# Kernel optimization log

Measured on AMD Instinct MI355X. Metric: run time of the kernel, lower is better.

The kernel has to match this reference:

```python
import jax, jax.numpy as jnp
import numpy as np

B, L, E, H = 4096, 200, 64, 128

def setup_inputs() -> dict:
    key = jax.random.key(0)
    k1, k2, k3, k4, k5, k6, k7 = jax.random.split(key, 7)
    behavior_emb = jax.random.normal(k1, (B, L, E), dtype=jnp.float32)
    target_emb = jax.random.normal(k2, (B, 1, E), dtype=jnp.float32)
    seq_len = jax.random.randint(k3, (B,), 0, 200)
    # attention MLP params: Linear(4E, H), Linear(H, 1)
    W1 = jax.random.normal(k4, (4 * E, H), dtype=jnp.float32) / np.sqrt(4 * E)
    b1 = jnp.zeros((H,), dtype=jnp.float32)
    W2 = jax.random.normal(k5, (H, 1), dtype=jnp.float32) / np.sqrt(H)
    b2 = jnp.zeros((1,), dtype=jnp.float32)
    return {"behavior_emb": behavior_emb, "target_emb": target_emb,
            "seq_len": seq_len, "W1": W1, "b1": b1, "W2": W2, "b2": b2}

def reference(behavior_emb, target_emb, seq_len, W1, b1, W2, b2):
    b, l, e = behavior_emb.shape
    t = jnp.broadcast_to(target_emb, (b, l, e))  # [B,L,E]
    # concat(behavior, target, behavior*target, behavior-target) -> [B,L,4E]
    feat = jnp.concatenate([behavior_emb, t, behavior_emb * t, behavior_emb - t], axis=-1)
    h = jax.nn.relu(jnp.einsum('blf,fh->blh', feat, W1) + b1)  # dropout = identity (eval)
    att = (jnp.einsum('blh,ho->blo', h, W2) + b2)[..., 0]      # [B,L]
    mask = jnp.arange(l)[None, :] < seq_len[:, None]           # [B,L]
    att = jnp.where(mask, att, -1e9)
    att = jax.nn.softmax(att, axis=-1)
    weighted_emb = jnp.einsum('bl,ble->be', att, behavior_emb)  # [B,E]
    return weighted_emb
```

## Files before the change

kernel.cpp:

```cpp
#include <hip/hip_runtime.h>
#include <hip/hip_bf16.h>

typedef __attribute__((ext_vector_type(8))) __bf16 bf16x8;
typedef __attribute__((ext_vector_type(4))) __bf16 bf16x4;
typedef __attribute__((ext_vector_type(4))) float  f32x4;

#define L_SEQ 200
#define LPAD  208

__global__ __launch_bounds__(256) void din_attn_kernel(
    const float* __restrict__ behavior,
    const float* __restrict__ target,
    const int*   __restrict__ seqlen,
    const float* __restrict__ W1,
    const float* __restrict__ b1,
    const float* __restrict__ W2,
    float* __restrict__ out)
{
    __shared__ __align__(16) __bf16 Xbf[LPAD * 64];
    __shared__ __align__(16) __bf16 Wb[128 * 64];
    __shared__ float t_s[64];
    __shared__ float tb_s[128];
    __shared__ float att_s[L_SEQ];
    __shared__ float red_s[8];
    __shared__ float part_s[4 * 64];

    const int b    = blockIdx.x;
    const int tid  = threadIdx.x;
    const int lane = tid & 63;
    const int wave = tid >> 6;

    if (tid < 64) t_s[tid] = target[b * 64 + tid];
    __syncthreads();

    {
        const int col = tid & 127;
        const int kh  = tid >> 7;
        #pragma unroll
        for (int kk = 0; kk < 32; ++kk) {
            const int k = kh * 32 + kk;
            float w = W1[k * 128 + col] + W1[(192 + k) * 128 + col]
                    + t_s[k] * W1[(128 + k) * 128 + col];
            Wb[col * 64 + (k ^ ((col & 7) << 3))] = (__bf16)w;
        }
    }
    if (tid < 128) {
        float acc = b1[tid];
        #pragma unroll 4
        for (int e = 0; e < 64; ++e)
            acc += t_s[e] * (W1[(64 + e) * 128 + tid] - W1[(192 + e) * 128 + tid]);
        tb_s[tid] = acc;
    }
    {
        const float4* Xg = (const float4*)(behavior + (size_t)b * L_SEQ * 64);
        for (int q = tid; q < L_SEQ * 16; q += 256) {
            const int row = q >> 4;
            const int j   = q & 15;
            float4 v = Xg[q];
            const int idx = row * 64 + ((j * 4) ^ ((row & 7) << 3));
            bf16x4 u = { (__bf16)v.x, (__bf16)v.y, (__bf16)v.z, (__bf16)v.w };
            *(bf16x4*)&Xbf[idx] = u;
        }
        for (int q = tid; q < 8 * 64; q += 256) {
            const int row = L_SEQ + (q >> 6);
            const int e   = q & 63;
            Xbf[row * 64 + (e ^ ((row & 7) << 3))] = (__bf16)0.0f;
        }
    }
    __syncthreads();

    {
        bf16x8 bfrag[8][2];
        float tb_l[8], w2_l[8];
        #pragma unroll
        for (int nt = 0; nt < 8; ++nt) {
            const int col = nt * 16 + (lane & 15);
            #pragma unroll
            for (int ks = 0; ks < 2; ++ks) {
                const int k0 = ks * 32 + (lane >> 4) * 8;
                bfrag[nt][ks] = *(const bf16x8*)&Wb[col * 64 + (k0 ^ ((col & 7) << 3))];
            }
            tb_l[nt] = tb_s[col];
            w2_l[nt] = W2[col];
        }
        const f32x4 zero = {0.f, 0.f, 0.f, 0.f};
        for (int tile = wave; tile < 13; tile += 4) {
            const int row = tile * 16 + (lane & 15);
            const int k0  = (lane >> 4) * 8;
            const int sw  = (row & 7) << 3;
            bf16x8 a0 = *(const bf16x8*)&Xbf[row * 64 + (k0 ^ sw)];
            bf16x8 a1 = *(const bf16x8*)&Xbf[row * 64 + ((k0 + 32) ^ sw)];
            f32x4 acc[8];
            #pragma unroll
            for (int nt = 0; nt < 8; ++nt) acc[nt] = zero;
            #pragma unroll
            for (int nt = 0; nt < 8; ++nt) {
                acc[nt] = __builtin_amdgcn_mfma_f32_16x16x32_bf16(a0, bfrag[nt][0], acc[nt], 0, 0, 0);
                acc[nt] = __builtin_amdgcn_mfma_f32_16x16x32_bf16(a1, bfrag[nt][1], acc[nt], 0, 0, 0);
            }
            float s[4] = {0.f, 0.f, 0.f, 0.f};
            #pragma unroll
            for (int nt = 0; nt < 8; ++nt) {
                #pragma unroll
                for (int i = 0; i < 4; ++i)
                    s[i] += fmaxf(acc[nt][i] + tb_l[nt], 0.f) * w2_l[nt];
            }
            #pragma unroll
            for (int i = 0; i < 4; ++i) {
                float v = s[i];
                v += __shfl_xor(v, 1, 64);
                v += __shfl_xor(v, 2, 64);
                v += __shfl_xor(v, 4, 64);
                v += __shfl_xor(v, 8, 64);
                s[i] = v;
            }
            if ((lane & 15) == 0) {
                const int r = tile * 16 + (lane >> 4) * 4;
                #pragma unroll
                for (int i = 0; i < 4; ++i)
                    if (r + i < L_SEQ) att_s[r + i] = s[i];
            }
        }
    }
    __syncthreads();

    {
        const int sl = seqlen[b];
        float val = -INFINITY;
        if (tid < L_SEQ) val = (tid < sl) ? att_s[tid] : -1e9f;
        float m = val;
        #pragma unroll
        for (int d = 1; d < 64; d <<= 1) m = fmaxf(m, __shfl_xor(m, d, 64));
        if (lane == 0) red_s[wave] = m;
        __syncthreads();
        m = fmaxf(fmaxf(red_s[0], red_s[1]), fmaxf(red_s[2], red_s[3]));
        float p = (tid < L_SEQ) ? __expf(val - m) : 0.f;
        float sum = p;
        #pragma unroll
        for (int d = 1; d < 64; d <<= 1) sum += __shfl_xor(sum, d, 64);
        if (lane == 0) red_s[4 + wave] = sum;
        __syncthreads();
        sum = red_s[4] + red_s[5] + red_s[6] + red_s[7];
        const float winv = 1.0f / sum;
        if (tid < L_SEQ) att_s[tid] = p * winv;
    }
    __syncthreads();

    {
        float acc = 0.f;
        for (int l = wave; l < L_SEQ; l += 4)
            acc += att_s[l] * (float)Xbf[l * 64 + (lane ^ ((l & 7) << 3))];
        part_s[wave * 64 + lane] = acc;
    }
    __syncthreads();
    if (tid < 64)
        out[(size_t)b * 64 + tid] =
            part_s[tid] + part_s[64 + tid] + part_s[128 + tid] + part_s[192 + tid];
}

extern "C" void kernel_launch(void* const* d_in, const int* in_sizes, int n_in,
                              void* d_out, int out_size, void* d_ws, size_t ws_size,
                              hipStream_t stream) {
    (void)n_in; (void)out_size; (void)d_ws; (void)ws_size;
    const float* behavior = (const float*)d_in[0];
    const float* target   = (const float*)d_in[1];
    const int*   seqlen   = (const int*)d_in[2];
    const float* W1       = (const float*)d_in[3];
    const float* b1       = (const float*)d_in[4];
    const float* W2       = (const float*)d_in[5];
    float* out = (float*)d_out;
    const int B = in_sizes[2];
    din_attn_kernel<<<dim3(B), dim3(256), 0, stream>>>(behavior, target, seqlen, W1, b1, W2, out);
}
```

Before: 389.3 us.

## Precompute batch-independent weight fragments and per-batch bias in separate setup kernels

Moves the per-block folding of W1 into a shared bf16 weight matrix out to a one-time setup kernel that writes MFMA-ready fragments. The target-dependent bias is computed by a second batched setup kernel. The main kernel now forms the behavior*target operand on the fly, running a K=128 GEMM split across waves by column tile, with per-wave partial scores summed in shared memory. This removes redundant W1 reads and the shared weight buffer from every block, which should raise occupancy. The cost is two extra launches, a workspace dependency, more MFMA work per tile, and bf16 rounding of the product and bias.

New measurement: 334.2 us. -14.1%, faster.

```diff
diff --git a/kernel.cpp b/kernel.cpp
--- a/kernel.cpp
+++ b/kernel.cpp
@@ -8,58 +8,105 @@
 #define L_SEQ 200
 #define LPAD  208
 
-__global__ __launch_bounds__(256) void din_attn_kernel(
+__global__ void setup_bc(const float* __restrict__ W1, __bf16* __restrict__ Bc) {
+    const int idx = blockIdx.x * 256 + threadIdx.x;
+    const int j  = idx & 7;
+    const int c  = (idx >> 3) & 15;
+    const int kq = (idx >> 7) & 3;
+    const int ks = (idx >> 9) & 3;
+    const int ct = idx >> 11;
+    const int k   = ks * 32 + kq * 8 + j;
+    const int col = ct * 16 + c;
+    float v;
+    if (k < 64) v = W1[k * 128 + col] + W1[(192 + k) * 128 + col];
+    else        v = W1[(128 + (k - 64)) * 128 + col];
+    Bc[idx] = (__bf16)v;
+}
+
+__global__ __launch_bounds__(256) void setup_tb(
+    const float* __restrict__ target, const float* __restrict__ W1,
+    const float* __restrict__ b1, __bf16* __restrict__ TB)
+{
+    __shared__ float Wbd[64][128];
+    __shared__ float Ts[16][64];
+    const int tid = threadIdx.x;
+    const int b0  = blockIdx.x * 16;
+    for (int q = tid; q < 64 * 128; q += 256) {
+        const int e = q >> 7, c = q & 127;
+        Wbd[e][c] = W1[(64 + e) * 128 + c] - W1[(192 + e) * 128 + c];
+    }
+    for (int q = tid; q < 16 * 64; q += 256) {
+        const int bb = q >> 6, e = q & 63;
+        Ts[bb][e] = target[(size_t)(b0 + bb) * 64 + e];
+    }
+    __syncthreads();
+    const int bb = tid >> 4;
+    const int c0 = (tid & 15) * 8;
+    float acc[8];
+    #pragma unroll
+    for (int r = 0; r < 8; ++r) acc[r] = b1[c0 + r];
+    for (int e = 0; e < 64; ++e) {
+        const float tv = Ts[bb][e];
+        #pragma unroll
+        for (int r = 0; r < 8; ++r) acc[r] += tv * Wbd[e][c0 + r];
+    }
+    #pragma unroll
+    for (int r = 0; r < 8; ++r)
+        TB[(size_t)(b0 + bb) * 128 + c0 + r] = (__bf16)acc[r];
+}
+
+__global__ __launch_bounds__(256, 4) void din_main(
     const float* __restrict__ behavior,
     const float* __restrict__ target,
     const int*   __restrict__ seqlen,
-    const float* __restrict__ W1,
-    const float* __restrict__ b1,
     const float* __restrict__ W2,
+    const __bf16* __restrict__ Bc,
+    const __bf16* __restrict__ TB,
     float* __restrict__ out)
 {
     __shared__ __align__(16) __bf16 Xbf[LPAD * 64];
-    __shared__ __align__(16) __bf16 Wb[128 * 64];
-    __shared__ float t_s[64];
-    __shared__ float tb_s[128];
-    __shared__ float att_s[L_SEQ];
+    __shared__ float att_part[4][LPAD];
+    __shared__ float att_s[LPAD];
     __shared__ float red_s[8];
     __shared__ float part_s[4 * 64];
 
     const int b    = blockIdx.x;
     const int tid  = threadIdx.x;
     const int lane = tid & 63;
-    const int wave = tid >> 6;
-
-    if (tid < 64) t_s[tid] = target[b * 64 + tid];
-    __syncthreads();
-
-    {
-        const int col = tid & 127;
-        const int kh  = tid >> 7;
-        #pragma unroll
-        for (int kk = 0; kk < 32; ++kk) {
-            const int k = kh * 32 + kk;
-            float w = W1[k * 128 + col] + W1[(192 + k) * 128 + col]
-                    + t_s[k] * W1[(128 + k) * 128 + col];
-            Wb[col * 64 + (k ^ ((col & 7) << 3))] = (__bf16)w;
-        }
-    }
-    if (tid < 128) {
-        float acc = b1[tid];
-        #pragma unroll 4
-        for (int e = 0; e < 64; ++e)
-            acc += t_s[e] * (W1[(64 + e) * 128 + tid] - W1[(192 + e) * 128 + tid]);
-        tb_s[tid] = acc;
-    }
+    const int w    = tid >> 6;
+    const int kq   = lane >> 4;
+    const int c16  = lane & 15;
+
+    bf16x8 bfrag[2][4];
+    #pragma unroll
+    for (int i = 0; i < 2; ++i) {
+        const int ct = 2 * w + i;
+        #pragma unroll
+        for (int ks = 0; ks < 4; ++ks)
+            bfrag[i][ks] = *(const bf16x8*)(Bc + ((ct * 4 + ks) * 4 + kq) * 128 + c16 * 8);
+    }
+    float tf0[8], tf1[8];
+    {
+        const float* tp = target + (size_t)b * 64 + kq * 8;
+        #pragma unroll
+        for (int j = 0; j < 8; ++j) { tf0[j] = tp[j]; tf1[j] = tp[32 + j]; }
+    }
+    float tb_l[2], w2_l[2];
+    #pragma unroll
+    for (int i = 0; i < 2; ++i) {
+        const int col = (2 * w + i) * 16 + c16;
+        tb_l[i] = (float)TB[(size_t)b * 128 + col];
+        w2_l[i] = W2[col];
+    }
+
     {
         const float4* Xg = (const float4*)(behavior + (size_t)b * L_SEQ * 64);
         for (int q = tid; q < L_SEQ * 16; q += 256) {
             const int row = q >> 4;
             const int j   = q & 15;
             float4 v = Xg[q];
-            const int idx = row * 64 + ((j * 4) ^ ((row & 7) << 3));
             bf16x4 u = { (__bf16)v.x, (__bf16)v.y, (__bf16)v.z, (__bf16)v.w };
-            *(bf16x4*)&Xbf[idx] = u;
+            *(bf16x4*)&Xbf[row * 64 + ((j * 4) ^ ((row & 7) << 3))] = u;
         }
         for (int q = tid; q < 8 * 64; q += 256) {
             const int row = L_SEQ + (q >> 6);
@@ -70,55 +117,43 @@
     __syncthreads();
 
     {
-        bf16x8 bfrag[8][2];
-        float tb_l[8], w2_l[8];
-        #pragma unroll
-        for (int nt = 0; nt < 8; ++nt) {
-            const int col = nt * 16 + (lane & 15);
-            #pragma unroll
-            for (int ks = 0; ks < 2; ++ks) {
-                const int k0 = ks * 32 + (lane >> 4) * 8;
-                bfrag[nt][ks] = *(const bf16x8*)&Wb[col * 64 + (k0 ^ ((col & 7) << 3))];
-            }
-            tb_l[nt] = tb_s[col];
-            w2_l[nt] = W2[col];
-        }
-        const f32x4 zero = {0.f, 0.f, 0.f, 0.f};
-        for (int tile = wave; tile < 13; tile += 4) {
-            const int row = tile * 16 + (lane & 15);
-            const int k0  = (lane >> 4) * 8;
+        const int k0 = kq * 8;
+        for (int tile = 0; tile < 13; ++tile) {
+            const int row = tile * 16 + c16;
             const int sw  = (row & 7) << 3;
             bf16x8 a0 = *(const bf16x8*)&Xbf[row * 64 + (k0 ^ sw)];
             bf16x8 a1 = *(const bf16x8*)&Xbf[row * 64 + ((k0 + 32) ^ sw)];
-            f32x4 acc[8];
+            bf16x8 a2, a3;
             #pragma unroll
-            for (int nt = 0; nt < 8; ++nt) acc[nt] = zero;
-            #pragma unroll
-            for (int nt = 0; nt < 8; ++nt) {
-                acc[nt] = __builtin_amdgcn_mfma_f32_16x16x32_bf16(a0, bfrag[nt][0], acc[nt], 0, 0, 0);
-                acc[nt] = __builtin_amdgcn_mfma_f32_16x16x32_bf16(a1, bfrag[nt][1], acc[nt], 0, 0, 0);
+            for (int j = 0; j < 8; ++j) {
+                a2[j] = (__bf16)((float)a0[j] * tf0[j]);
+                a3[j] = (__bf16)((float)a1[j] * tf1[j]);
             }
             float s[4] = {0.f, 0.f, 0.f, 0.f};
             #pragma unroll
-            for (int nt = 0; nt < 8; ++nt) {
+            for (int i = 0; i < 2; ++i) {
+                f32x4 acc = {0.f, 0.f, 0.f, 0.f};
+                acc = __builtin_amdgcn_mfma_f32_16x16x32_bf16(a0, bfrag[i][0], acc, 0, 0, 0);
+                acc = __builtin_amdgcn_mfma_f32_16x16x32_bf16(a1, bfrag[i][1], acc, 0, 0, 0);
+                acc = __builtin_amdgcn_mfma_f32_16x16x32_bf16(a2, bfrag[i][2], acc, 0, 0, 0);
+                acc = __builtin_amdgcn_mfma_f32_16x16x32_bf16(a3, bfrag[i][3], acc, 0, 0, 0);
                 #pragma unroll
-                for (int i = 0; i < 4; ++i)
-                    s[i] += fmaxf(acc[nt][i] + tb_l[nt], 0.f) * w2_l[nt];
+                for (int r = 0; r < 4; ++r)
+                    s[r] += fmaxf(acc[r] + tb_l[i], 0.f) * w2_l[i];
             }
             #pragma unroll
-            for (int i = 0; i < 4; ++i) {
-                float v = s[i];
+            for (int r = 0; r < 4; ++r) {
+                float v = s[r];
                 v += __shfl_xor(v, 1, 64);
                 v += __shfl_xor(v, 2, 64);
                 v += __shfl_xor(v, 4, 64);
                 v += __shfl_xor(v, 8, 64);
-                s[i] = v;
-            }
-            if ((lane & 15) == 0) {
-                const int r = tile * 16 + (lane >> 4) * 4;
+                s[r] = v;
+            }
+            if (c16 == 0) {
+                const int r0 = tile * 16 + kq * 4;
                 #pragma unroll
-                for (int i = 0; i < 4; ++i)
-                    if (r + i < L_SEQ) att_s[r + i] = s[i];
+                for (int r = 0; r < 4; ++r) att_part[w][r0 + r] = s[r];
             }
         }
     }
@@ -127,18 +162,22 @@
     {
         const int sl = seqlen[b];
         float val = -INFINITY;
-        if (tid < L_SEQ) val = (tid < sl) ? att_s[tid] : -1e9f;
+        if (tid < L_SEQ) {
+            float v = att_part[0][tid] + att_part[1][tid]
+                    + att_part[2][tid] + att_part[3][tid];
+            val = (tid < sl) ? v : -1e9f;
+        }
         float m = val;
         #pragma unroll
         for (int d = 1; d < 64; d <<= 1) m = fmaxf(m, __shfl_xor(m, d, 64));
-        if (lane == 0) red_s[wave] = m;
+        if (lane == 0) red_s[w] = m;
         __syncthreads();
         m = fmaxf(fmaxf(red_s[0], red_s[1]), fmaxf(red_s[2], red_s[3]));
         float p = (tid < L_SEQ) ? __expf(val - m) : 0.f;
         float sum = p;
         #pragma unroll
         for (int d = 1; d < 64; d <<= 1) sum += __shfl_xor(sum, d, 64);
-        if (lane == 0) red_s[4 + wave] = sum;
+        if (lane == 0) red_s[4 + w] = sum;
         __syncthreads();
         sum = red_s[4] + red_s[5] + red_s[6] + red_s[7];
         const float winv = 1.0f / sum;
@@ -148,9 +187,9 @@
 
     {
         float acc = 0.f;
-        for (int l = wave; l < L_SEQ; l += 4)
+        for (int l = w; l < L_SEQ; l += 4)
             acc += att_s[l] * (float)Xbf[l * 64 + (lane ^ ((l & 7) << 3))];
-        part_s[wave * 64 + lane] = acc;
+        part_s[w * 64 + lane] = acc;
     }
     __syncthreads();
     if (tid < 64)
@@ -161,7 +200,7 @@
 extern "C" void kernel_launch(void* const* d_in, const int* in_sizes, int n_in,
                               void* d_out, int out_size, void* d_ws, size_t ws_size,
                               hipStream_t stream) {
-    (void)n_in; (void)out_size; (void)d_ws; (void)ws_size;
+    (void)n_in; (void)out_size; (void)ws_size;
     const float* behavior = (const float*)d_in[0];
     const float* target   = (const float*)d_in[1];
     const int*   seqlen   = (const int*)d_in[2];
@@ -170,5 +209,11 @@
     const float* W2       = (const float*)d_in[5];
     float* out = (float*)d_out;
     const int B = in_sizes[2];
-    din_attn_kernel<<<dim3(B), dim3(256), 0, stream>>>(behavior, target, seqlen, W1, b1, W2, out);
-}
+
+    __bf16* Bc = (__bf16*)d_ws;
+    __bf16* TB = (__bf16*)((char*)d_ws + 32768);
+
+    setup_bc<<<dim3(64), dim3(256), 0, stream>>>(W1, Bc);
+    setup_tb<<<dim3(B / 16), dim3(256), 0, stream>>>(target, W1, b1, TB);
+    din_main<<<dim3(B), dim3(256), 0, stream>>>(behavior, target, seqlen, W2, Bc, TB, out);
+}
```
